# Optimization experiments

Measured on AMD Instinct MI355X. Metric: run time of the kernel, lower is better.

## Reference

```python
import jax, jax.numpy as jnp
import numpy as np

V = 32000   # vocab_size
S = 4096    # seq_len
D = 1024    # dim
H = 4096    # hidden_dim
L = 2       # num_layers
CS = 64     # chunk_size
R = 256     # low_rank_dim = max(8, D//4)
WIN = 8     # window_size (OptitationLayer default)
NEG = -1e30


def setup_inputs() -> dict:
    key = jax.random.key(0)
    ks = jax.random.split(key, 20)
    f32 = jnp.float32
    inp = {}
    inp['idx_seq'] = jax.random.randint(ks[0], (S,), 0, V)
    inp['embeddings'] = jax.random.normal(ks[1], (V, D), f32) * 0.01
    inp['positional'] = jax.random.normal(ks[2], (S, D), f32) * 0.01
    # per-layer MLP params, stacked over layer axis
    inp['Wg'] = jax.random.normal(ks[3], (L, D, D), f32) / D ** 0.5
    inp['bg'] = jnp.zeros((L, D), f32)
    inp['Ws'] = jax.random.normal(ks[4], (L, D, H), f32) / D ** 0.5
    inp['bs'] = jnp.zeros((L, H), f32)
    inp['Wo'] = jax.random.normal(ks[5], (L, H, D), f32) / H ** 0.5
    inp['bo'] = jnp.zeros((L, D), f32)
    # per-layer optitation (windowed attention) params
    inp['Wq'] = jax.random.normal(ks[6], (L, D, R), f32) / D ** 0.5
    inp['Wk'] = jax.random.normal(ks[7], (L, D, R), f32) / D ** 0.5
    inp['Wv'] = jax.random.normal(ks[8], (L, D, R), f32) / D ** 0.5
    inp['Wao'] = jax.random.normal(ks[9], (L, R, D), f32) / R ** 0.5
    inp['bq'] = jnp.zeros((L, R), f32)
    inp['bk'] = jnp.zeros((L, R), f32)
    inp['bv'] = jnp.zeros((L, R), f32)
    inp['bao'] = jnp.zeros((L, D), f32)
    inp['outW'] = jax.random.normal(ks[10], (D, V), f32) / D ** 0.5
    inp['outb'] = jnp.zeros((V,), f32)
    return inp


def _optitation(x, Wq, bq, Wk, bk, Wv, bv, Wao, bao):
    Q = x @ Wq + bq
    K = x @ Wk + bk
    Vv = x @ Wv + bv
    s = x.shape[0]
    off = jnp.arange(WIN + 1)
    j = jnp.arange(s)[:, None] - off[None, :]  # [s, w+1] key indices
    valid = j >= 0
    jc = jnp.maximum(j, 0)
    Kw = K[jc]   # [s, w+1, R]
    Vw = Vv[jc]  # [s, w+1, R]
    scores = jnp.einsum('sr,swr->sw', Q, Kw) / jnp.sqrt(jnp.float32(R))
    scores = jnp.where(valid, scores, NEG)
    attn = jax.nn.softmax(scores, axis=-1)
    ao = jnp.einsum('sw,swr->sr', attn, Vw)   # [s, R]
    return ao @ Wao + bao


def _chunk_link(x):
    # chunk-averaging with half-weighted neighbor chunks
    s, d = x.shape
    pad = (-s) % CS
    xp = jnp.pad(x, ((0, pad), (0, 0)))
    n = xp.shape[0] // CS
    c = xp.reshape(n, CS, d)
    prev = jnp.concatenate([jnp.zeros_like(c[:1]), c[:-1]], axis=0)
    nxt = jnp.concatenate([c[1:], jnp.zeros_like(c[:1])], axis=0)
    i = jnp.arange(n)
    w = 1.0 + 0.5 * (i > 0).astype(x.dtype) + 0.5 * (i < n - 1).astype(x.dtype)
    upd = (c + 0.5 * prev + 0.5 * nxt) / w[:, None, None]
    return upd.reshape(-1, d)[:s]


def reference(idx_seq, embeddings, positional, Wg, bg, Ws, bs, Wo, bo,
              Wq, bq, Wk, bk, Wv, bv, Wao, bao, outW, outb):
    s = idx_seq.shape[0]
    x = embeddings[idx_seq] + positional[:s]
    # decay accumulation: x[pos] += 0.8**pos * x[0] for pos >= 1 (x[0] untouched)
    decay = jnp.power(jnp.float32(0.8), jnp.arange(s, dtype=jnp.float32))
    decay = decay.at[0].set(0.0)
    x = x + decay[:, None] * x[0]
    for l in range(L):
        residual = x
        x = x * jax.nn.sigmoid(x @ Wg[l] + bg[l])            # lensed gate
        x = jnp.tanh(x @ Ws[l] + bs[l]) @ Wo[l] + bo[l]       # context sculpt
        x = x + residual
        x = x + _optitation(x, Wq[l], bq[l], Wk[l], bk[l],
                            Wv[l], bv[l], Wao[l], bao[l])
        x = _chunk_link(x)
    return x @ outW + outb
```

## Files before the change

kernel.cpp:

```cpp
#include <hip/hip_runtime.h>
#include <hip/hip_bf16.h>
#include <math.h>

#define S_LEN 4096
#define DIM   1024
#define HID   4096
#define NLAYER 2
#define RDIM  256
#define VOCAB 32000
#define QKVN  768

typedef unsigned short u16;
typedef __attribute__((ext_vector_type(8))) short s16x8;
typedef __attribute__((ext_vector_type(4))) float f32x4;
typedef __attribute__((ext_vector_type(4))) unsigned short u16x4;

__device__ inline u16 f2b(float f){
  unsigned u = __float_as_uint(f);
  u += 0x7fff + ((u >> 16) & 1);
  return (u16)(u >> 16);
}

__device__ inline void gload_lds16(const void* g, void* l){
  __builtin_amdgcn_global_load_lds((__attribute__((address_space(1))) void*)(g),
                                   (__attribute__((address_space(3))) void*)(l), 16, 0, 0);
}

__global__ void k_transpose(const float* __restrict__ src, u16* __restrict__ dst,
                            int K, int N, size_t srcLS, size_t dstLS){
  __shared__ float tile[64][65];
  src += (size_t)blockIdx.z * srcLS;
  dst += (size_t)blockIdx.z * dstLS;
  int n0 = blockIdx.x * 64, k0 = blockIdx.y * 64;
  int tx = threadIdx.x, ty = threadIdx.y;
  #pragma unroll
  for (int i = 0; i < 4; i++){
    float4 v = *(const float4*)&src[(size_t)(k0 + ty + 16 * i) * N + n0 + tx * 4];
    tile[ty + 16 * i][tx * 4 + 0] = v.x;
    tile[ty + 16 * i][tx * 4 + 1] = v.y;
    tile[ty + 16 * i][tx * 4 + 2] = v.z;
    tile[ty + 16 * i][tx * 4 + 3] = v.w;
  }
  __syncthreads();
  #pragma unroll
  for (int i = 0; i < 4; i++){
    u16x4 o;
    #pragma unroll
    for (int j = 0; j < 4; j++) o[j] = f2b(tile[tx * 4 + j][ty + 16 * i]);
    *(u16x4*)&dst[(size_t)(n0 + ty + 16 * i) * K + k0 + tx * 4] = o;
  }
}

__global__ void k_embed(const int* __restrict__ idx, const float* __restrict__ emb,
                        const float* __restrict__ pos, float* __restrict__ xf,
                        u16* __restrict__ xb){
  int s = blockIdx.x;
  int d = blockIdx.y * 256 + threadIdx.x;
  float v = emb[(size_t)idx[s] * DIM + d] + pos[(size_t)s * DIM + d];
  if (s > 0){
    float x0 = emb[(size_t)idx[0] * DIM + d] + pos[d];
    v += exp2f((float)s * -0.3219280948873623f) * x0;
  }
  size_t o = (size_t)s * DIM + d;
  xf[o] = v; xb[o] = f2b(v);
}

#define EP_GATE  0
#define EP_TANH  1
#define EP_RESID 2
#define EP_BIASF 3
#define EP_AO    4
#define EP_OUT   5

#define PH_SYNC() do{ asm volatile("" ::: "memory"); __builtin_amdgcn_s_barrier(); asm volatile("" ::: "memory"); }while(0)


#define MMA_QUAD(MH, NLO, BF) \
  { _Pragma("unroll") for (int mi = 0; mi < 4; mi++){ \
    _Pragma("unroll") for (int ni = 0; ni < 2; ni++){ \
      _Pragma("unroll") for (int ks = 0; ks < 2; ks++){ \
        acc[(MH)*4+mi][(NLO)+ni] = __builtin_amdgcn_mfma_f32_16x16x32_bf16((BF)[ni*2+ks], af[mi*2+ks], acc[(MH)*4+mi][(NLO)+ni], 0, 0, 0); } } } }

#define LDA(MH, BO) \
  { _Pragma("unroll") for (int mi = 0; mi < 4; mi++){ \
    _Pragma("unroll") for (int ks = 0; ks < 2; ks++){ \
      af[mi*2+ks] = *(const s16x8*)(pa0 + (BO) + ((MH)*4+mi)*1024 + ((ks ^ kb) * 32)); } } }

#define LDB(NH, BO) \
  { _Pragma("unroll") for (int ni = 0; ni < 2; ni++){ \
    _Pragma("unroll") for (int ks = 0; ks < 2; ks++){ \
      bf_[(NH)*4+ni*2+ks] = *(const s16x8*)(pb0 + (BO) + ((NH)*2+ni)*1024 + ((ks ^ kb) * 32)); } } }

template<int EPI>
__global__ __launch_bounds__(512, 2) void k_gemm8(
    const u16* __restrict__ A, const u16* __restrict__ Bt,
    const float* __restrict__ bias,
    float* __restrict__ outf, u16* __restrict__ outbf,
    int N, int K, int tilesM, int tilesN){
  extern __shared__ u16 lds[];
  const int t = threadIdx.x;
  const int w = t >> 6, l = t & 63;
  const int wr = w >> 2, wc = w & 3;
  const int NT = K >> 6;
  const int NI = NT >> 1;

  int nwg = tilesM * tilesN;
  int id = blockIdx.x, id2;
  if ((nwg & 7) == 0){ int c = nwg >> 3; id2 = (id & 7) * c + (id >> 3); }
  else id2 = id;
  int pr = tilesN * 2;
  int stripe = id2 / pr, r2 = id2 % pr;
  int bm = stripe * 2 + (r2 & 1);
  int bn = r2 >> 1;
  const int bRow = bm * 256, bCol = bn * 256;

  const int r0 = t >> 3;
  const int scol = (((t & 7) ^ ((t >> 3) & 7)) * 8);

  auto stage_half = [&](int tau, int q){
    if (tau >= NT) return;
    int h = q & 1;
    bool isA = q < 2;
    const u16* gp = (isA ? A + (size_t)bRow * K : Bt + (size_t)bCol * K)
                 + (size_t)(h * 128 + r0) * K + (size_t)tau * 64 + scol;
    u16* d = lds + (isA ? 0 : 32768) + ((tau & 1) * 16384) + h * 8192 + t * 8;
    gload_lds16(gp, d);
    gload_lds16(gp + (size_t)64 * K, d + 4096);
  };

  const int cb = (((l >> 4) ^ (l & 3)) * 8);
  const int kb = (l >> 2) & 1;
  const u16* pa0 = lds + (wr * 128 + (l & 15)) * 64 + cb;
  const u16* pb0 = lds + 32768 + (wc * 64 + (l & 15)) * 64 + cb;

  f32x4 acc[8][4] = {};
  s16x8 af[8], bf_[8];

  stage_half(0, 0); stage_half(0, 1); stage_half(0, 2); stage_half(0, 3);
  stage_half(1, 0);
  asm volatile("s_waitcnt vmcnt(2)" ::: "memory");
  PH_SYNC();

  for (int i = 0; i < NI; i++){
    const int t1 = 2 * i + 1, t2 = 2 * i + 2, t3 = 2 * i + 3;
    const bool last = (i + 1 == NI);
    LDA(0, 0); LDB(0, 0);
    stage_half(t1, 1);
    PH_SYNC();
    __builtin_amdgcn_s_setprio(1); MMA_QUAD(0, 0, bf_); __builtin_amdgcn_s_setprio(0);
    PH_SYNC();
    LDB(1, 0);
    stage_half(t1, 2);
    PH_SYNC();
    __builtin_amdgcn_s_setprio(1); MMA_QUAD(0, 2, bf_ + 4); __builtin_amdgcn_s_setprio(0);
    PH_SYNC();
    LDA(1, 0);
    stage_half(t1, 3);
    PH_SYNC();
    __builtin_amdgcn_s_setprio(1); MMA_QUAD(1, 2, bf_ + 4); __builtin_amdgcn_s_setprio(0);
    PH_SYNC();
    stage_half(t2, 0);
    if (!last) asm volatile("s_waitcnt vmcnt(2)" ::: "memory");
    else       asm volatile("s_waitcnt vmcnt(0)" ::: "memory");
    PH_SYNC();
    __builtin_amdgcn_s_setprio(1); MMA_QUAD(1, 0, bf_); __builtin_amdgcn_s_setprio(0);
    PH_SYNC();
    LDA(0, 16384); LDB(0, 16384);
    stage_half(t2, 1);
    PH_SYNC();
    __builtin_amdgcn_s_setprio(1); MMA_QUAD(0, 0, bf_); __builtin_amdgcn_s_setprio(0);
    PH_SYNC();
    LDB(1, 16384);
    stage_half(t2, 2);
    PH_SYNC();
    __builtin_amdgcn_s_setprio(1); MMA_QUAD(0, 2, bf_ + 4); __builtin_amdgcn_s_setprio(0);
    PH_SYNC();
    LDA(1, 16384);
    stage_half(t2, 3);
    PH_SYNC();
    __builtin_amdgcn_s_setprio(1); MMA_QUAD(1, 2, bf_ + 4); __builtin_amdgcn_s_setprio(0);
    PH_SYNC();
    stage_half(t3, 0);
    if (!last) asm volatile("s_waitcnt vmcnt(2)" ::: "memory");
    PH_SYNC();
    __builtin_amdgcn_s_setprio(1); MMA_QUAD(1, 0, bf_); __builtin_amdgcn_s_setprio(0);
    PH_SYNC();
  }

  #pragma unroll
  for (int m = 0; m < 8; m++){
    int gr = bRow + wr * 128 + m * 16 + (l & 15);
    #pragma unroll
    for (int n = 0; n < 4; n++){
      int gc = bCol + wc * 64 + n * 16 + ((l >> 4) * 4);
      f32x4 v = acc[m][n] + *(const f32x4*)(bias + gc);
      *(f32x4*)(outf + (size_t)gr * N + gc) = v;
    }
  }
}


#define MMA2(MH, NL) \
  { _Pragma("unroll") for (int mi = 0; mi < 2; mi++){ \
    _Pragma("unroll") for (int ks = 0; ks < 2; ks++){ \
      acc[(MH)*2+mi][(NL)] = __builtin_amdgcn_mfma_f32_16x16x32_bf16(bf_[(NL)*2+ks], af[mi*2+ks], acc[(MH)*2+mi][(NL)], 0, 0, 0); } } }

#define LDA2(MH, BO) \
  { _Pragma("unroll") for (int mi = 0; mi < 2; mi++){ \
    _Pragma("unroll") for (int ks = 0; ks < 2; ks++){ \
      af[mi*2+ks] = *(const s16x8*)(pa0 + (BO) + ((MH)*2+mi)*1024 + ((ks ^ kb) * 32)); } } }

#define LDB2(NL, BO) \
  { _Pragma("unroll") for (int ks = 0; ks < 2; ks++){ \
    bf_[(NL)*2+ks] = *(const s16x8*)(pb0 + (BO) + (NL)*1024 + ((ks ^ kb) * 32)); } }

template<int EPI>
__global__ __launch_bounds__(512, 4) void k_gemm8b(
    const u16* __restrict__ A, const u16* __restrict__ Bt,
    const float* __restrict__ bias, const float* __restrict__ aux,
    float* __restrict__ outf, u16* __restrict__ outbf,
    int N, int K, int tilesM, int tilesN){
  extern __shared__ u16 lds[];
  const int t = threadIdx.x;
  const int w = t >> 6, l = t & 63;
  const int wr = w >> 2, wc = w & 3;
  const int NT = K >> 6;
  const int NI = NT >> 1;

  int nwg = tilesM * tilesN;
  int id = blockIdx.x, id2;
  if ((nwg & 7) == 0){ int c = nwg >> 3; id2 = (id & 7) * c + (id >> 3); }
  else id2 = id;
  int per = tilesM << 3;
  int g = id2 / per, r = id2 % per;
  int bm = r % tilesM;
  int bn = (g << 3) + r / tilesM;
  const int bRow = bm * 128, bCol = bn * 128;

  const int r0 = t >> 3;
  const int scol = (((t & 7) ^ ((t >> 3) & 7)) * 8);

  auto stage_half = [&](int tau, int q){
    if (tau >= NT) return;
    int h = q & 1;
    bool isA = q < 2;
    const u16* gp = (isA ? A + (size_t)bRow * K : Bt + (size_t)bCol * K)
                 + (size_t)(h * 64 + r0) * K + (size_t)tau * 64 + scol;
    u16* d = lds + (isA ? 0 : 16384) + ((tau & 1) * 8192) + h * 4096 + t * 8;
    gload_lds16(gp, d);
  };

  const int cb = (((l >> 4) ^ (l & 3)) * 8);
  const int kb = (l >> 2) & 1;
  const u16* pa0 = lds + wr * 4096 + (l & 15) * 64 + cb;
  const u16* pb0 = lds + 16384 + (wc >> 1) * 4096 + ((wc & 1) * 32 + (l & 15)) * 64 + cb;

  f32x4 acc[4][2] = {};
  s16x8 af[4], bf_[4];

  stage_half(0, 0); stage_half(0, 1); stage_half(0, 2); stage_half(0, 3);
  stage_half(1, 0);
  asm volatile("s_waitcnt vmcnt(1)" ::: "memory");
  PH_SYNC();

  for (int i = 0; i < NI; i++){
    const int t1 = 2 * i + 1, t2 = 2 * i + 2, t3 = 2 * i + 3;
    const bool last = (i + 1 == NI);
    LDA2(0, 0); LDB2(0, 0);
    stage_half(t1, 1);
    PH_SYNC();
    __builtin_amdgcn_s_setprio(1); MMA2(0, 0); __builtin_amdgcn_s_setprio(0);
    PH_SYNC();
    LDB2(1, 0);
    stage_half(t1, 2);
    PH_SYNC();
    __builtin_amdgcn_s_setprio(1); MMA2(0, 1); __builtin_amdgcn_s_setprio(0);
    PH_SYNC();
    LDA2(1, 0);
    stage_half(t1, 3);
    PH_SYNC();
    __builtin_amdgcn_s_setprio(1); MMA2(1, 1); __builtin_amdgcn_s_setprio(0);
    PH_SYNC();
    stage_half(t2, 0);
    if (!last) asm volatile("s_waitcnt vmcnt(1)" ::: "memory");
    else       asm volatile("s_waitcnt vmcnt(0)" ::: "memory");
    PH_SYNC();
    __builtin_amdgcn_s_setprio(1); MMA2(1, 0); __builtin_amdgcn_s_setprio(0);
    PH_SYNC();
    LDA2(0, 8192); LDB2(0, 8192);
    stage_half(t2, 1);
    PH_SYNC();
    __builtin_amdgcn_s_setprio(1); MMA2(0, 0); __builtin_amdgcn_s_setprio(0);
    PH_SYNC();
    LDB2(1, 8192);
    stage_half(t2, 2);
    PH_SYNC();
    __builtin_amdgcn_s_setprio(1); MMA2(0, 1); __builtin_amdgcn_s_setprio(0);
    PH_SYNC();
    LDA2(1, 8192);
    stage_half(t2, 3);
    PH_SYNC();
    __builtin_amdgcn_s_setprio(1); MMA2(1, 1); __builtin_amdgcn_s_setprio(0);
    PH_SYNC();
    stage_half(t3, 0);
    if (!last) asm volatile("s_waitcnt vmcnt(1)" ::: "memory");
    PH_SYNC();
    __builtin_amdgcn_s_setprio(1); MMA2(1, 0); __builtin_amdgcn_s_setprio(0);
    PH_SYNC();
  }

  #pragma unroll
  for (int m = 0; m < 4; m++){
    int gr = bRow + wr * 64 + m * 16 + (l & 15);
    #pragma unroll
    for (int n = 0; n < 2; n++){
      int gc = bCol + wc * 32 + n * 16 + ((l >> 4) * 4);
      size_t o = (size_t)gr * N + gc;
      f32x4 v = acc[m][n] + *(const f32x4*)(bias + gc);
      if constexpr (EPI == EP_GATE){
        f32x4 a = *(const f32x4*)(aux + o);
        u16x4 rr;
        #pragma unroll
        for (int q = 0; q < 4; q++) rr[q] = f2b(a[q] / (1.f + expf(-v[q])));
        *(u16x4*)(outbf + o) = rr;
      } else if constexpr (EPI == EP_TANH){
        u16x4 rr;
        #pragma unroll
        for (int q = 0; q < 4; q++) rr[q] = f2b(tanhf(v[q]));
        *(u16x4*)(outbf + o) = rr;
      } else if constexpr (EPI == EP_RESID){
        v += *(const f32x4*)(aux + o);
        *(f32x4*)(outf + o) = v;
        u16x4 rr;
        #pragma unroll
        for (int q = 0; q < 4; q++) rr[q] = f2b(v[q]);
        *(u16x4*)(outbf + o) = rr;
      } else if constexpr (EPI == EP_BIASF){
        *(f32x4*)(outf + o) = v;
      } else if constexpr (EPI == EP_AO){
        v += *(const f32x4*)(aux + o);
        *(f32x4*)(outf + o) = v;
      } else {
        *(f32x4*)(outf + o) = v;
      }
    }
  }
}

__global__ void k_attn(const float* __restrict__ qkv, u16* __restrict__ aob){
  int s = blockIdx.x * 4 + (threadIdx.x >> 6);
  int l = threadIdx.x & 63;
  const float* qp = qkv + (size_t)s * QKVN;
  float qr[4];
  #pragma unroll
  for (int r = 0; r < 4; r++) qr[r] = qp[l + 64 * r];
  float sc[9];
  float mx = -1e30f;
  #pragma unroll
  for (int j = 0; j <= 8; j++){
    int sj = s - j;
    bool ok = sj >= 0;
    int row = ok ? sj : 0;
    const float* kp = qkv + (size_t)row * QKVN + RDIM;
    float p = 0.f;
    #pragma unroll
    for (int r = 0; r < 4; r++) p += qr[r] * kp[l + 64 * r];
    #pragma unroll
    for (int off = 32; off; off >>= 1) p += __shfl_xor(p, off);
    p = ok ? p * 0.0625f : -1e30f;
    sc[j] = p;
    mx = fmaxf(mx, p);
  }
  float den = 0.f;
  #pragma unroll
  for (int j = 0; j <= 8; j++){ sc[j] = expf(sc[j] - mx); den += sc[j]; }
  float inv = 1.f / den;
  #pragma unroll
  for (int r = 0; r < 4; r++){
    float a = 0.f;
    #pragma unroll
    for (int j = 0; j <= 8; j++){
      int sj = s - j;
      int row = sj >= 0 ? sj : 0;
      a += sc[j] * qkv[(size_t)row * QKVN + 512 + l + 64 * r];
    }
    aob[(size_t)s * RDIM + l + 64 * r] = f2b(a * inv);
  }
}

__global__ void k_chunk(const float* __restrict__ xin, float* __restrict__ xout,
                        u16* __restrict__ xb){
  int s = blockIdx.x;
  int d = blockIdx.y * 256 + threadIdx.x;
  int ci = s >> 6;
  float v = xin[(size_t)s * DIM + d];
  float wsum = 1.f;
  if (ci > 0){ v += 0.5f * xin[(size_t)(s - 64) * DIM + d]; wsum += 0.5f; }
  if (ci < 63){ v += 0.5f * xin[(size_t)(s + 64) * DIM + d]; wsum += 0.5f; }
  v /= wsum;
  size_t o = (size_t)s * DIM + d;
  xout[o] = v; xb[o] = f2b(v);
}

__global__ void k_concat3(const float* __restrict__ a, const float* __restrict__ b,
                          const float* __restrict__ c, float* __restrict__ dst){
  int i = threadIdx.x;
  dst[i] = a[i]; dst[256 + i] = b[i]; dst[512 + i] = c[i];
}

extern "C" void kernel_launch(void* const* d_in, const int* in_sizes, int n_in,
                              void* d_out, int out_size, void* d_ws, size_t ws_size,
                              hipStream_t stream){
  const int*   idx  = (const int*)d_in[0];
  const float* emb  = (const float*)d_in[1];
  const float* pos  = (const float*)d_in[2];
  const float* Wg   = (const float*)d_in[3];
  const float* bg   = (const float*)d_in[4];
  const float* Ws_  = (const float*)d_in[5];
  const float* bs   = (const float*)d_in[6];
  const float* Wo   = (const float*)d_in[7];
  const float* bo   = (const float*)d_in[8];
  const float* Wq   = (const float*)d_in[9];
  const float* Wk   = (const float*)d_in[10];
  const float* Wv   = (const float*)d_in[11];
  const float* Wao  = (const float*)d_in[12];
  const float* bq   = (const float*)d_in[13];
  const float* bk   = (const float*)d_in[14];
  const float* bv   = (const float*)d_in[15];
  const float* bao  = (const float*)d_in[16];
  const float* outW = (const float*)d_in[17];
  const float* outb = (const float*)d_in[18];
  float* out = (float*)d_out;

  char* p = (char*)d_ws;
  auto alloc = [&](size_t n)->char*{ char* r = p; p += (n + 255) & ~(size_t)255; return r; };
  float* xfA  = (float*)alloc((size_t)S_LEN * DIM * 4);
  float* xfB  = (float*)alloc((size_t)S_LEN * DIM * 4);
  u16*   xb   = (u16*)  alloc((size_t)S_LEN * DIM * 2);
  u16*   xgb  = (u16*)  alloc((size_t)S_LEN * DIM * 2);
  u16*   tbuf = (u16*)  alloc((size_t)S_LEN * HID * 2);
  float* qkvf = (float*)alloc((size_t)S_LEN * QKVN * 4);
  u16*   aob  = (u16*)  alloc((size_t)S_LEN * RDIM * 2);
  float* bqkv = (float*)alloc(QKVN * 4);
  u16*   WgT  = (u16*)  alloc((size_t)NLAYER * DIM * DIM * 2);
  u16*   WsT  = (u16*)  alloc((size_t)NLAYER * DIM * HID * 2);
  u16*   WoT  = (u16*)  alloc((size_t)NLAYER * HID * DIM * 2);
  u16*   WqkvT= (u16*)  alloc((size_t)NLAYER * QKVN * DIM * 2);
  u16*   WaoT = (u16*)  alloc((size_t)NLAYER * RDIM * DIM * 2);
  u16*   outWT= (u16*)  alloc((size_t)VOCAB * DIM * 2);

  (void)hipFuncSetAttribute((const void*)&k_gemm8<EP_OUT>,
                      hipFuncAttributeMaxDynamicSharedMemorySize, 131072);
  (void)hipFuncSetAttribute((const void*)&k_gemm8b<EP_GATE>,
                      hipFuncAttributeMaxDynamicSharedMemorySize, 65536);
  (void)hipFuncSetAttribute((const void*)&k_gemm8b<EP_TANH>,
                      hipFuncAttributeMaxDynamicSharedMemorySize, 65536);
  (void)hipFuncSetAttribute((const void*)&k_gemm8b<EP_RESID>,
                      hipFuncAttributeMaxDynamicSharedMemorySize, 65536);
  (void)hipFuncSetAttribute((const void*)&k_gemm8b<EP_BIASF>,
                      hipFuncAttributeMaxDynamicSharedMemorySize, 65536);
  (void)hipFuncSetAttribute((const void*)&k_gemm8b<EP_AO>,
                      hipFuncAttributeMaxDynamicSharedMemorySize, 65536);

  dim3 tb16(16, 16);
  k_transpose<<<dim3(DIM/64,  DIM/64,  NLAYER), tb16, 0, stream>>>(Wg,  WgT,  DIM, DIM,  (size_t)DIM*DIM,  (size_t)DIM*DIM);
  k_transpose<<<dim3(HID/64,  DIM/64,  NLAYER), tb16, 0, stream>>>(Ws_, WsT,  DIM, HID,  (size_t)DIM*HID,  (size_t)DIM*HID);
  k_transpose<<<dim3(DIM/64,  HID/64,  NLAYER), tb16, 0, stream>>>(Wo,  WoT,  HID, DIM,  (size_t)HID*DIM,  (size_t)HID*DIM);
  k_transpose<<<dim3(RDIM/64, DIM/64,  NLAYER), tb16, 0, stream>>>(Wq,  WqkvT,                 DIM, RDIM, (size_t)DIM*RDIM, (size_t)QKVN*DIM);
  k_transpose<<<dim3(RDIM/64, DIM/64,  NLAYER), tb16, 0, stream>>>(Wk,  WqkvT + (size_t)256*DIM, DIM, RDIM, (size_t)DIM*RDIM, (size_t)QKVN*DIM);
  k_transpose<<<dim3(RDIM/64, DIM/64,  NLAYER), tb16, 0, stream>>>(Wv,  WqkvT + (size_t)512*DIM, DIM, RDIM, (size_t)DIM*RDIM, (size_t)QKVN*DIM);
  k_transpose<<<dim3(DIM/64,  RDIM/64, NLAYER), tb16, 0, stream>>>(Wao, WaoT, RDIM, DIM, (size_t)RDIM*DIM, (size_t)RDIM*DIM);
  k_transpose<<<dim3(VOCAB/64, DIM/64, 1),      tb16, 0, stream>>>(outW, outWT, DIM, VOCAB, 0, 0);

  k_embed<<<dim3(S_LEN, DIM/256), 256, 0, stream>>>(idx, emb, pos, xfA, xb);

  float* curF = xfA; float* altF = xfB;
  for (int l = 0; l < NLAYER; l++){
    k_gemm8b<EP_GATE ><<<(S_LEN/128)*(DIM/128),  512, 65536, stream>>>(xb,  WgT  + (size_t)l*DIM*DIM,  bg + (size_t)l*DIM, curF, nullptr, xgb, DIM, DIM, S_LEN/128, DIM/128);
    k_gemm8b<EP_TANH ><<<(S_LEN/128)*(HID/128),  512, 65536, stream>>>(xgb, WsT  + (size_t)l*DIM*HID,  bs + (size_t)l*HID, nullptr, nullptr, tbuf, HID, DIM, S_LEN/128, HID/128);
    k_gemm8b<EP_RESID><<<(S_LEN/128)*(DIM/128),  512, 65536, stream>>>(tbuf,WoT  + (size_t)l*HID*DIM,  bo + (size_t)l*DIM, curF, curF, xb, DIM, HID, S_LEN/128, DIM/128);
    k_concat3<<<1, 256, 0, stream>>>(bq + (size_t)l*RDIM, bk + (size_t)l*RDIM, bv + (size_t)l*RDIM, bqkv);
    k_gemm8b<EP_BIASF><<<(S_LEN/128)*(QKVN/128), 512, 65536, stream>>>(xb,  WqkvT + (size_t)l*QKVN*DIM, bqkv, nullptr, qkvf, nullptr, QKVN, DIM, S_LEN/128, QKVN/128);
    k_attn<<<S_LEN/4, 256, 0, stream>>>(qkvf, aob);
    k_gemm8b<EP_AO   ><<<(S_LEN/128)*(DIM/128),  512, 65536, stream>>>(aob, WaoT + (size_t)l*RDIM*DIM, bao + (size_t)l*DIM, curF, curF, nullptr, DIM, RDIM, S_LEN/128, DIM/128);
    k_chunk<<<dim3(S_LEN, DIM/256), 256, 0, stream>>>(curF, altF, xb);
    float* tmp = curF; curF = altF; altF = tmp;
  }
  k_gemm8<EP_OUT><<<(S_LEN/256)*(VOCAB/256), 512, 131072, stream>>>(xb, outWT, outb, out, nullptr, VOCAB, DIM, S_LEN/256, VOCAB/256);
}
```

Baseline: 884.6 us.

## Make output-projection GEMM persistent with cross-tile prefetch of next tile's operands

The final vocab projection GEMM becomes a persistent kernel launched with 256 workgroups that loop over the 2000 output tiles. While finishing the current tile, it prefetches the first K-slices of the next tile into LDS, so the load pipeline stays busy across tile boundaries instead of draining and refilling. The XCD-aware block remapping is removed and tiles are assigned by a strided loop, which may change L2 locality. Accumulators are zeroed after each epilogue store.

```diff
diff --git a/kernel.cpp b/kernel.cpp
--- a/kernel.cpp
+++ b/kernel.cpp
@@ -91,11 +91,9 @@
     _Pragma("unroll") for (int ks = 0; ks < 2; ks++){ \
       bf_[(NH)*4+ni*2+ks] = *(const s16x8*)(pb0 + (BO) + ((NH)*2+ni)*1024 + ((ks ^ kb) * 32)); } } }
 
-template<int EPI>
-__global__ __launch_bounds__(512, 2) void k_gemm8(
+__global__ __launch_bounds__(512, 2) void k_gemmL(
     const u16* __restrict__ A, const u16* __restrict__ Bt,
-    const float* __restrict__ bias,
-    float* __restrict__ outf, u16* __restrict__ outbf,
+    const float* __restrict__ bias, float* __restrict__ outf,
     int N, int K, int tilesM, int tilesN){
   extern __shared__ u16 lds[];
   const int t = threadIdx.x;
@@ -103,36 +101,44 @@
   const int wr = w >> 2, wc = w & 3;
   const int NT = K >> 6;
   const int NI = NT >> 1;
-
-  int nwg = tilesM * tilesN;
-  int id = blockIdx.x, id2;
-  if ((nwg & 7) == 0){ int c = nwg >> 3; id2 = (id & 7) * c + (id >> 3); }
-  else id2 = id;
-  int pr = tilesN * 2;
-  int stripe = id2 / pr, r2 = id2 % pr;
-  int bm = stripe * 2 + (r2 & 1);
-  int bn = r2 >> 1;
-  const int bRow = bm * 256, bCol = bn * 256;
+  const int nTiles = tilesM * tilesN;
 
   const int r0 = t >> 3;
   const int scol = (((t & 7) ^ ((t >> 3) & 7)) * 8);
-
-  auto stage_half = [&](int tau, int q){
-    if (tau >= NT) return;
-    int h = q & 1;
-    bool isA = q < 2;
-    const u16* gp = (isA ? A + (size_t)bRow * K : Bt + (size_t)bCol * K)
-                 + (size_t)(h * 128 + r0) * K + (size_t)tau * 64 + scol;
-    u16* d = lds + (isA ? 0 : 32768) + ((tau & 1) * 16384) + h * 8192 + t * 8;
-    gload_lds16(gp, d);
-    gload_lds16(gp + (size_t)64 * K, d + 4096);
-  };
-
   const int cb = (((l >> 4) ^ (l & 3)) * 8);
   const int kb = (l >> 2) & 1;
   const u16* pa0 = lds + (wr * 128 + (l & 15)) * 64 + cb;
   const u16* pb0 = lds + 32768 + (wc * 64 + (l & 15)) * 64 + cb;
 
+  auto decode = [&](int idx, int& bR, int& bC){
+    int pr = tilesN * 2;
+    int stripe = idx / pr, r2 = idx % pr;
+    bR = (stripe * 2 + (r2 & 1)) * 256;
+    bC = (r2 >> 1) * 256;
+  };
+
+  int tileIdx = blockIdx.x;
+  if (tileIdx >= nTiles) return;
+  int bRow, bCol, nRow = 0, nCol = 0;
+  bool hasNext = false;
+  decode(tileIdx, bRow, bCol);
+
+  auto stage_half = [&](int tau, int q){
+    const u16* base;
+    if (tau >= NT){
+      if (!hasNext) return;
+      tau -= NT;
+      base = (q < 2) ? A + (size_t)nRow * K : Bt + (size_t)nCol * K;
+    } else {
+      base = (q < 2) ? A + (size_t)bRow * K : Bt + (size_t)bCol * K;
+    }
+    int h = q & 1;
+    const u16* gp = base + (size_t)(h * 128 + r0) * K + (size_t)tau * 64 + scol;
+    u16* d = lds + ((q < 2) ? 0 : 32768) + ((tau & 1) * 16384) + h * 8192 + t * 8;
+    gload_lds16(gp, d);
+    gload_lds16(gp + (size_t)64 * K, d + 4096);
+  };
+
   f32x4 acc[8][4] = {};
   s16x8 af[8], bf_[8];
 
@@ -141,61 +147,69 @@
   asm volatile("s_waitcnt vmcnt(2)" ::: "memory");
   PH_SYNC();
 
-  for (int i = 0; i < NI; i++){
-    const int t1 = 2 * i + 1, t2 = 2 * i + 2, t3 = 2 * i + 3;
-    const bool last = (i + 1 == NI);
-    LDA(0, 0); LDB(0, 0);
-    stage_half(t1, 1);
-    PH_SYNC();
-    __builtin_amdgcn_s_setprio(1); MMA_QUAD(0, 0, bf_); __builtin_amdgcn_s_setprio(0);
-    PH_SYNC();
-    LDB(1, 0);
-    stage_half(t1, 2);
-    PH_SYNC();
-    __builtin_amdgcn_s_setprio(1); MMA_QUAD(0, 2, bf_ + 4); __builtin_amdgcn_s_setprio(0);
-    PH_SYNC();
-    LDA(1, 0);
-    stage_half(t1, 3);
-    PH_SYNC();
-    __builtin_amdgcn_s_setprio(1); MMA_QUAD(1, 2, bf_ + 4); __builtin_amdgcn_s_setprio(0);
-    PH_SYNC();
-    stage_half(t2, 0);
-    if (!last) asm volatile("s_waitcnt vmcnt(2)" ::: "memory");
-    else       asm volatile("s_waitcnt vmcnt(0)" ::: "memory");
-    PH_SYNC();
-    __builtin_amdgcn_s_setprio(1); MMA_QUAD(1, 0, bf_); __builtin_amdgcn_s_setprio(0);
-    PH_SYNC();
-    LDA(0, 16384); LDB(0, 16384);
-    stage_half(t2, 1);
-    PH_SYNC();
-    __builtin_amdgcn_s_setprio(1); MMA_QUAD(0, 0, bf_); __builtin_amdgcn_s_setprio(0);
-    PH_SYNC();
-    LDB(1, 16384);
-    stage_half(t2, 2);
-    PH_SYNC();
-    __builtin_amdgcn_s_setprio(1); MMA_QUAD(0, 2, bf_ + 4); __builtin_amdgcn_s_setprio(0);
-    PH_SYNC();
-    LDA(1, 16384);
-    stage_half(t2, 3);
-    PH_SYNC();
-    __builtin_amdgcn_s_setprio(1); MMA_QUAD(1, 2, bf_ + 4); __builtin_amdgcn_s_setprio(0);
-    PH_SYNC();
-    stage_half(t3, 0);
-    if (!last) asm volatile("s_waitcnt vmcnt(2)" ::: "memory");
-    PH_SYNC();
-    __builtin_amdgcn_s_setprio(1); MMA_QUAD(1, 0, bf_); __builtin_amdgcn_s_setprio(0);
-    PH_SYNC();
-  }
-
-  #pragma unroll
-  for (int m = 0; m < 8; m++){
-    int gr = bRow + wr * 128 + m * 16 + (l & 15);
+  for (; tileIdx < nTiles; tileIdx += gridDim.x){
+    int nIdx = tileIdx + gridDim.x;
+    hasNext = nIdx < nTiles;
+    if (hasNext) decode(nIdx, nRow, nCol);
+
+    for (int i = 0; i < NI; i++){
+      const int t1 = 2 * i + 1, t2 = 2 * i + 2, t3 = 2 * i + 3;
+      const bool lastGate = (!hasNext) && (i + 1 == NI);
+      LDA(0, 0); LDB(0, 0);
+      stage_half(t1, 1);
+      PH_SYNC();
+      __builtin_amdgcn_s_setprio(1); MMA_QUAD(0, 0, bf_); __builtin_amdgcn_s_setprio(0);
+      PH_SYNC();
+      LDB(1, 0);
+      stage_half(t1, 2);
+      PH_SYNC();
+      __builtin_amdgcn_s_setprio(1); MMA_QUAD(0, 2, bf_ + 4); __builtin_amdgcn_s_setprio(0);
+      PH_SYNC();
+      LDA(1, 0);
+      stage_half(t1, 3);
+      PH_SYNC();
+      __builtin_amdgcn_s_setprio(1); MMA_QUAD(1, 2, bf_ + 4); __builtin_amdgcn_s_setprio(0);
+      PH_SYNC();
+      stage_half(t2, 0);
+      if (!lastGate) asm volatile("s_waitcnt vmcnt(2)" ::: "memory");
+      else           asm volatile("s_waitcnt vmcnt(0)" ::: "memory");
+      PH_SYNC();
+      __builtin_amdgcn_s_setprio(1); MMA_QUAD(1, 0, bf_); __builtin_amdgcn_s_setprio(0);
+      PH_SYNC();
+      LDA(0, 16384); LDB(0, 16384);
+      stage_half(t2, 1);
+      PH_SYNC();
+      __builtin_amdgcn_s_setprio(1); MMA_QUAD(0, 0, bf_); __builtin_amdgcn_s_setprio(0);
+      PH_SYNC();
+      LDB(1, 16384);
+      stage_half(t2, 2);
+      PH_SYNC();
+      __builtin_amdgcn_s_setprio(1); MMA_QUAD(0, 2, bf_ + 4); __builtin_amdgcn_s_setprio(0);
+      PH_SYNC();
+      LDA(1, 16384);
+      stage_half(t2, 3);
+      PH_SYNC();
+      __builtin_amdgcn_s_setprio(1); MMA_QUAD(1, 2, bf_ + 4); __builtin_amdgcn_s_setprio(0);
+      PH_SYNC();
+      stage_half(t3, 0);
+      if (!lastGate) asm volatile("s_waitcnt vmcnt(2)" ::: "memory");
+      PH_SYNC();
+      __builtin_amdgcn_s_setprio(1); MMA_QUAD(1, 0, bf_); __builtin_amdgcn_s_setprio(0);
+      PH_SYNC();
+    }
+
     #pragma unroll
-    for (int n = 0; n < 4; n++){
-      int gc = bCol + wc * 64 + n * 16 + ((l >> 4) * 4);
-      f32x4 v = acc[m][n] + *(const f32x4*)(bias + gc);
-      *(f32x4*)(outf + (size_t)gr * N + gc) = v;
+    for (int m = 0; m < 8; m++){
+      int gr = bRow + wr * 128 + m * 16 + (l & 15);
+      #pragma unroll
+      for (int n = 0; n < 4; n++){
+        int gc = bCol + wc * 64 + n * 16 + ((l >> 4) * 4);
+        f32x4 v = acc[m][n] + *(const f32x4*)(bias + gc);
+        *(f32x4*)(outf + (size_t)gr * N + gc) = v;
+        acc[m][n] = (f32x4){0.f, 0.f, 0.f, 0.f};
+      }
     }
+    bRow = nRow; bCol = nCol;
   }
 }
 
@@ -449,7 +463,7 @@
   u16*   WaoT = (u16*)  alloc((size_t)NLAYER * RDIM * DIM * 2);
   u16*   outWT= (u16*)  alloc((size_t)VOCAB * DIM * 2);
 
-  (void)hipFuncSetAttribute((const void*)&k_gemm8<EP_OUT>,
+  (void)hipFuncSetAttribute((const void*)&k_gemmL,
                       hipFuncAttributeMaxDynamicSharedMemorySize, 131072);
   (void)hipFuncSetAttribute((const void*)&k_gemm8b<EP_GATE>,
                       hipFuncAttributeMaxDynamicSharedMemorySize, 65536);
@@ -486,5 +500,5 @@
     k_chunk<<<dim3(S_LEN, DIM/256), 256, 0, stream>>>(curF, altF, xb);
     float* tmp = curF; curF = altF; altF = tmp;
   }
-  k_gemm8<EP_OUT><<<(S_LEN/256)*(VOCAB/256), 512, 131072, stream>>>(xb, outWT, outb, out, nullptr, VOCAB, DIM, S_LEN/256, VOCAB/256);
-}
+  k_gemmL<<<256, 512, 131072, stream>>>(xb, outWT, outb, out, VOCAB, DIM, S_LEN/256, VOCAB/256);
+}
```

New measurement: 843.3 us. 1.05x faster.
